# Performance work log

Measured on AMD Instinct MI355X. Metric: run time of the kernel, lower is better.

Reference implementation:

```python
import jax, jax.numpy as jnp
import numpy as np

N = 50000
E = 800000
IN_CH, HID, OUT_CH = 8, 64, 1
NEG_SLOPE = 0.2


def setup_inputs() -> dict:
    key = jax.random.key(0)
    ks = jax.random.split(key, 16)
    x = jax.random.normal(ks[0], (N, IN_CH), dtype=jnp.float32)
    edge_index = jax.random.randint(ks[1], (2, E), 0, N, dtype=jnp.int64)
    def glorot(k, shape):
        fan = shape[0] + shape[-1]
        return jax.random.uniform(k, shape, jnp.float32, -1.0, 1.0) * jnp.sqrt(6.0 / fan)
    # layer 1: in=8 -> 4 heads x 64, concat=False (mean over heads)
    W1 = glorot(ks[2], (IN_CH, 4 * HID))
    as1 = glorot(ks[3], (4, HID)); ad1 = glorot(ks[4], (4, HID))
    b1 = jnp.zeros((HID,), jnp.float32)
    # layer 2: 64 -> 4 heads x 64
    W2 = glorot(ks[5], (HID, 4 * HID))
    as2 = glorot(ks[6], (4, HID)); ad2 = glorot(ks[7], (4, HID))
    b2 = jnp.zeros((HID,), jnp.float32)
    # layer 3: 64 -> 1 head x 1
    W3 = glorot(ks[8], (HID, OUT_CH))
    as3 = glorot(ks[9], (1, OUT_CH)); ad3 = glorot(ks[10], (1, OUT_CH))
    b3 = jnp.zeros((OUT_CH,), jnp.float32)
    return {"x": x, "edge_index": edge_index,
            "W1": W1, "b1": b1, "as1": as1, "ad1": ad1,
            "W2": W2, "b2": b2, "as2": as2, "ad2": ad2,
            "W3": W3, "b3": b3, "as3": as3, "ad3": ad3}


def gat_conv(x, src, dst, W, b, a_src, a_dst, n_nodes):
    """PyG GATConv, concat=False (mean over heads), add_self_loops already applied."""
    heads, ch = a_src.shape
    h = (x @ W).reshape(n_nodes, heads, ch)            # [N,H,C]
    e_src = jnp.sum(h * a_src[None], axis=-1)          # [N,H]
    e_dst = jnp.sum(h * a_dst[None], axis=-1)          # [N,H]
    logits = jax.nn.leaky_relu(e_src[src] + e_dst[dst], NEG_SLOPE)  # [E,H]
    # softmax over incoming edges of each destination node (self loops ensure non-empty)
    m = jax.ops.segment_max(logits, dst, num_segments=n_nodes)      # [N,H]
    ex = jnp.exp(logits - m[dst])
    denom = jax.ops.segment_sum(ex, dst, num_segments=n_nodes)      # [N,H]
    alpha = ex / (denom[dst] + 1e-16)                  # [E,H]
    out = jax.ops.segment_sum(alpha[:, :, None] * h[src], dst, num_segments=n_nodes)  # [N,H,C]
    return jnp.mean(out, axis=1) + b                   # [N,C]


def reference(x, edge_index, W1, b1, as1, ad1, W2, b2, as2, ad2, W3, b3, as3, ad3):
    n = x.shape[0]
    loops = jnp.arange(n, dtype=edge_index.dtype)
    src = jnp.concatenate([edge_index[0], loops])
    dst = jnp.concatenate([edge_index[1], loops])
    h = jax.nn.elu(gat_conv(x, src, dst, W1, b1, as1, ad1, n))
    # Dropout(p=0.2) is identity in eval mode
    h = jax.nn.elu(gat_conv(h, src, dst, W2, b2, as2, ad2, n))
    out = jax.nn.sigmoid(gat_conv(h, src, dst, W3, b3, as3, ad3, n))
    return out  # [N,1] failure probability per node
```

## Files before the change

kernel.cpp:

```cpp
#include <hip/hip_runtime.h>
#include <hip/hip_bf16.h>
#include <hip/hip_fp16.h>
#include <math.h>

#define N_NODES 50000
#define N_EDGES 800000
#define N_TOT   (N_EDGES + N_NODES)
#define NEG_SLOPE 0.2f

static __device__ __forceinline__ float lrelu(float x){ return x >= 0.f ? x : NEG_SLOPE * x; }

__global__ void k_detect(const int* __restrict__ ei, int* __restrict__ flag){
  if (blockIdx.x == 0 && threadIdx.x == 0){
    int o = 0;
    #pragma unroll
    for (int i = 1; i < 16; i += 2) o |= ei[i];
    *flag = (o == 0) ? 1 : 0;
  }
}

__global__ void k_init(int* __restrict__ deg, int* __restrict__ fill){
  int i = blockIdx.x * blockDim.x + threadIdx.x;
  if (i < N_NODES){ deg[i] = 1; fill[i] = 0; }
}

__global__ void k_count(const int* __restrict__ ei, const int* __restrict__ flag,
                        int* __restrict__ deg){
  int e = blockIdx.x * blockDim.x + threadIdx.x;
  if (e >= N_EDGES) return;
  int f = *flag;
  int d = f ? ei[2*(N_EDGES + e)] : ei[N_EDGES + e];
  atomicAdd(&deg[d], 1);
}

__global__ void k_scan1(const int* __restrict__ deg, int* __restrict__ rowptr,
                        int* __restrict__ bsum){
  __shared__ int sd[256];
  int t = threadIdx.x;
  int base = blockIdx.x * 1024 + t * 4;
  int v0 = (base + 0 < N_NODES) ? deg[base + 0] : 0;
  int v1 = (base + 1 < N_NODES) ? deg[base + 1] : 0;
  int v2 = (base + 2 < N_NODES) ? deg[base + 2] : 0;
  int v3 = (base + 3 < N_NODES) ? deg[base + 3] : 0;
  int tsum = v0 + v1 + v2 + v3;
  sd[t] = tsum; __syncthreads();
  for (int off = 1; off < 256; off <<= 1){
    int vv = (t >= off) ? sd[t - off] : 0;
    __syncthreads();
    sd[t] += vv;
    __syncthreads();
  }
  int excl = sd[t] - tsum;
  if (base + 0 < N_NODES) rowptr[base + 0] = excl;
  if (base + 1 < N_NODES) rowptr[base + 1] = excl + v0;
  if (base + 2 < N_NODES) rowptr[base + 2] = excl + v0 + v1;
  if (base + 3 < N_NODES) rowptr[base + 3] = excl + v0 + v1 + v2;
  if (t == 255) bsum[blockIdx.x] = sd[255];
}

#define NB_SCAN 49
__global__ void k_scan2(const int* __restrict__ bsum, int* __restrict__ boff){
  int t = threadIdx.x;
  int v = (t < NB_SCAN) ? bsum[t] : 0;
  int incl = v;
  #pragma unroll
  for (int off = 1; off < 64; off <<= 1){
    int u = __shfl_up(incl, off);
    if (t >= off) incl += u;
  }
  if (t < NB_SCAN) boff[t] = incl - v;
}

__global__ void k_scan3(int* __restrict__ rowptr, const int* __restrict__ boff){
  int i = blockIdx.x * blockDim.x + threadIdx.x;
  if (i < N_NODES) rowptr[i] += boff[i >> 10];
  if (i == 0) rowptr[N_NODES] = N_TOT;
}

__global__ void k_scatter(const int* __restrict__ ei, const int* __restrict__ flag,
                          const int* __restrict__ rowptr, int* __restrict__ fill,
                          int* __restrict__ col){
  int e = blockIdx.x * blockDim.x + threadIdx.x;
  if (e >= N_TOT) return;
  int s, d;
  if (e < N_EDGES){
    int f = *flag;
    if (f){ s = ei[2*e]; d = ei[2*(N_EDGES + e)]; }
    else  { s = ei[e];   d = ei[N_EDGES + e]; }
  } else {
    s = d = e - N_EDGES;
  }
  int pos = atomicAdd(&fill[d], 1);
  col[rowptr[d] + pos] = s;
}


__global__ __launch_bounds__(256) void k_transform1(
    const float* __restrict__ xin, const float* __restrict__ W,
    const float* __restrict__ aS, const float* __restrict__ aD,
    __half* __restrict__ h, float* __restrict__ es, float* __restrict__ ed){
  __shared__ float wl[8 * 256];
  int tid = threadIdx.x;
  for (int i = tid; i < 8 * 256; i += 256) wl[i] = W[i];
  int lane = tid & 63, wv = tid >> 6, head = lane >> 4;
  float4 s4 = *(const float4*)&aS[4 * lane];
  float4 d4 = *(const float4*)&aD[4 * lane];
  __syncthreads();
  int base = (blockIdx.x * 4 + wv) * 8;
  for (int m = 0; m < 8; m++){
    int n = base + m;
    if (n >= N_NODES) break;
    float4 xa = *(const float4*)&xin[n * 8];
    float4 xb = *(const float4*)&xin[n * 8 + 4];
    float xs0 = xa.x, xs1 = xa.y, xs2 = xa.z, xs3 = xa.w;
    float xs4 = xb.x, xs5 = xb.y, xs6 = xb.z, xs7 = xb.w;
    float4 acc = make_float4(0.f, 0.f, 0.f, 0.f);
    #define T1STEP(k, xv) { float4 w4 = *(const float4*)&wl[(k)*256 + 4*lane]; \
      acc.x = fmaf(xv, w4.x, acc.x); acc.y = fmaf(xv, w4.y, acc.y); \
      acc.z = fmaf(xv, w4.z, acc.z); acc.w = fmaf(xv, w4.w, acc.w); }
    T1STEP(0, xs0) T1STEP(1, xs1) T1STEP(2, xs2) T1STEP(3, xs3)
    T1STEP(4, xs4) T1STEP(5, xs5) T1STEP(6, xs6) T1STEP(7, xs7)
    #undef T1STEP
    __half2 p0 = __floats2half2_rn(acc.x, acc.y);
    __half2 p1 = __floats2half2_rn(acc.z, acc.w);
    uint2 u; u.x = *(unsigned int*)&p0; u.y = *(unsigned int*)&p1;
    *(uint2*)&h[(size_t)n * 256 + 4 * lane] = u;
    float ps = acc.x*s4.x + acc.y*s4.y + acc.z*s4.z + acc.w*s4.w;
    float pd = acc.x*d4.x + acc.y*d4.y + acc.z*d4.z + acc.w*d4.w;
    #pragma unroll
    for (int off = 1; off < 16; off <<= 1){ ps += __shfl_xor(ps, off); pd += __shfl_xor(pd, off); }
    if ((lane & 15) == 0){ es[n * 4 + head] = ps; ed[n * 4 + head] = pd; }
  }
}

__global__ __launch_bounds__(256) void k_transform2(
    const float* __restrict__ xin, const float* __restrict__ W,
    const float* __restrict__ aS, const float* __restrict__ aD,
    __half* __restrict__ h, float* __restrict__ es, float* __restrict__ ed){
  __shared__ float wl[64 * 256];
  int tid = threadIdx.x;
  for (int i = tid; i < 64 * 256; i += 256) wl[i] = W[i];
  int lane = tid & 63, wv = tid >> 6, head = lane >> 4;
  float4 s4 = *(const float4*)&aS[4 * lane];
  float4 d4 = *(const float4*)&aD[4 * lane];
  __syncthreads();
  int base = (blockIdx.x * 4 + wv) * 8;
  float xr[8];
  #pragma unroll
  for (int m = 0; m < 8; m++){
    int n = base + m;
    xr[m] = (n < N_NODES) ? xin[(size_t)n * 64 + lane] : 0.f;
  }
  float4 acc[8];
  #pragma unroll
  for (int m = 0; m < 8; m++) acc[m] = make_float4(0.f, 0.f, 0.f, 0.f);
  #pragma unroll 4
  for (int k = 0; k < 64; k++){
    float4 w4 = *(const float4*)&wl[k * 256 + 4 * lane];
    #pragma unroll
    for (int m = 0; m < 8; m++){
      float xv = __shfl(xr[m], k);
      acc[m].x = fmaf(xv, w4.x, acc[m].x);
      acc[m].y = fmaf(xv, w4.y, acc[m].y);
      acc[m].z = fmaf(xv, w4.z, acc[m].z);
      acc[m].w = fmaf(xv, w4.w, acc[m].w);
    }
  }
  #pragma unroll
  for (int m = 0; m < 8; m++){
    int n = base + m;
    if (n >= N_NODES) break;
    __half2 p0 = __floats2half2_rn(acc[m].x, acc[m].y);
    __half2 p1 = __floats2half2_rn(acc[m].z, acc[m].w);
    uint2 u; u.x = *(unsigned int*)&p0; u.y = *(unsigned int*)&p1;
    *(uint2*)&h[(size_t)n * 256 + 4 * lane] = u;
    float ps = acc[m].x*s4.x + acc[m].y*s4.y + acc[m].z*s4.z + acc[m].w*s4.w;
    float pd = acc[m].x*d4.x + acc[m].y*d4.y + acc[m].z*d4.z + acc[m].w*d4.w;
    #pragma unroll
    for (int off = 1; off < 16; off <<= 1){ ps += __shfl_xor(ps, off); pd += __shfl_xor(pd, off); }
    if ((lane & 15) == 0){ es[n * 4 + head] = ps; ed[n * 4 + head] = pd; }
  }
}

__global__ __launch_bounds__(256) void k_transform3(
    const float* __restrict__ xin, const float* __restrict__ W3,
    const float* __restrict__ aS, const float* __restrict__ aD,
    float* __restrict__ h3, float* __restrict__ es3, float* __restrict__ ed3){
  int gid = blockIdx.x * blockDim.x + threadIdx.x;
  int n = gid >> 6, lane = gid & 63;
  if (n >= N_NODES) return;
  float v = xin[(size_t)n * 64 + lane] * W3[lane];
  #pragma unroll
  for (int off = 1; off < 64; off <<= 1) v += __shfl_xor(v, off);
  if (lane == 0){
    h3[n] = v;
    es3[n] = v * aS[0];
    ed3[n] = v * aD[0];
  }
}

__global__ __launch_bounds__(256) void k_agg(
    const __half* __restrict__ h, const float* __restrict__ es, const float* __restrict__ ed,
    const int* __restrict__ rowptr, const int* __restrict__ col,
    const float* __restrict__ bias, float* __restrict__ outf){
  int gid = blockIdx.x * blockDim.x + threadIdx.x;
  int d = gid >> 6, lane = gid & 63;
  if (d >= N_NODES) return;
  int start = rowptr[d], end = rowptr[d + 1];
  int head = lane >> 4;
  float eh = ed[d * 4 + head];
  const __half* hp = h + 4 * lane;
  float4 acc = make_float4(0.f, 0.f, 0.f, 0.f);
  float wsum = 0.f;
  int i = start;
  for (; i + 2 <= end; i += 2){
    int s0 = col[i], s1 = col[i + 1];
    float w0 = __expf(lrelu(es[s0 * 4 + head] + eh));
    float w1 = __expf(lrelu(es[s1 * 4 + head] + eh));
    uint2 u0 = *(const uint2*)(hp + (size_t)s0 * 256);
    uint2 u1 = *(const uint2*)(hp + (size_t)s1 * 256);
    wsum += w0 + w1;
    float2 a0 = __half22float2(*(__half2*)&u0.x);
    float2 b0 = __half22float2(*(__half2*)&u0.y);
    float2 a1 = __half22float2(*(__half2*)&u1.x);
    float2 b1 = __half22float2(*(__half2*)&u1.y);
    acc.x = fmaf(w0, a0.x, acc.x); acc.y = fmaf(w0, a0.y, acc.y);
    acc.z = fmaf(w0, b0.x, acc.z); acc.w = fmaf(w0, b0.y, acc.w);
    acc.x = fmaf(w1, a1.x, acc.x); acc.y = fmaf(w1, a1.y, acc.y);
    acc.z = fmaf(w1, b1.x, acc.z); acc.w = fmaf(w1, b1.y, acc.w);
  }
  if (i < end){
    int s0 = col[i];
    float w0 = __expf(lrelu(es[s0 * 4 + head] + eh));
    uint2 u0 = *(const uint2*)(hp + (size_t)s0 * 256);
    wsum += w0;
    float2 a0 = __half22float2(*(__half2*)&u0.x);
    float2 b0 = __half22float2(*(__half2*)&u0.y);
    acc.x = fmaf(w0, a0.x, acc.x); acc.y = fmaf(w0, a0.y, acc.y);
    acc.z = fmaf(w0, b0.x, acc.z); acc.w = fmaf(w0, b0.y, acc.w);
  }
  float inv = 1.0f / (wsum + 1e-16f);
  acc.x *= inv; acc.y *= inv; acc.z *= inv; acc.w *= inv;
  #pragma unroll
  for (int off = 16; off < 64; off <<= 1){
    acc.x += __shfl_xor(acc.x, off);
    acc.y += __shfl_xor(acc.y, off);
    acc.z += __shfl_xor(acc.z, off);
    acc.w += __shfl_xor(acc.w, off);
  }
  if (lane < 16){
    float4 b4 = *(const float4*)&bias[4 * lane];
    float ox = 0.25f * acc.x + b4.x;
    float oy = 0.25f * acc.y + b4.y;
    float oz = 0.25f * acc.z + b4.z;
    float ow = 0.25f * acc.w + b4.w;
    ox = ox > 0.f ? ox : expm1f(ox);
    oy = oy > 0.f ? oy : expm1f(oy);
    oz = oz > 0.f ? oz : expm1f(oz);
    ow = ow > 0.f ? ow : expm1f(ow);
    float4 o = make_float4(ox, oy, oz, ow);
    *(float4*)&outf[(size_t)d * 64 + 4 * lane] = o;
  }
}

__global__ __launch_bounds__(256) void k_agg3(
    const float* __restrict__ h3, const float* __restrict__ es3, const float* __restrict__ ed3,
    const int* __restrict__ rowptr, const int* __restrict__ col,
    const float* __restrict__ b3, float* __restrict__ out){
  int gid = blockIdx.x * blockDim.x + threadIdx.x;
  int d = gid >> 6, lane = gid & 63;
  if (d >= N_NODES) return;
  int start = rowptr[d], end = rowptr[d + 1];
  float edv = ed3[d];
  float num = 0.f, den = 0.f;
  for (int i = start + lane; i < end; i += 64){
    int s = col[i];
    float wgt = __expf(lrelu(es3[s] + edv));
    den += wgt;
    num = fmaf(wgt, h3[s], num);
  }
  #pragma unroll
  for (int off = 1; off < 64; off <<= 1){
    num += __shfl_xor(num, off);
    den += __shfl_xor(den, off);
  }
  if (lane == 0){
    float v = num / (den + 1e-16f) + b3[0];
    out[d] = 1.f / (1.f + __expf(-v));
  }
}

extern "C" void kernel_launch(void* const* d_in, const int* in_sizes, int n_in,
                              void* d_out, int out_size, void* d_ws, size_t ws_size,
                              hipStream_t stream) {
  const float* x   = (const float*)d_in[0];
  const int*   ei  = (const int*)  d_in[1];
  const float* W1  = (const float*)d_in[2];
  const float* b1  = (const float*)d_in[3];
  const float* as1 = (const float*)d_in[4];
  const float* ad1 = (const float*)d_in[5];
  const float* W2  = (const float*)d_in[6];
  const float* b2  = (const float*)d_in[7];
  const float* as2 = (const float*)d_in[8];
  const float* ad2 = (const float*)d_in[9];
  const float* W3  = (const float*)d_in[10];
  const float* b3  = (const float*)d_in[11];
  const float* as3 = (const float*)d_in[12];
  const float* ad3 = (const float*)d_in[13];
  float* out = (float*)d_out;

  char* w = (char*)d_ws;
  size_t off = 0;
  auto alloc = [&](size_t bytes) -> char* {
    char* p = w + off;
    off += (bytes + 255) & ~size_t(255);
    return p;
  };
  int*    flag   = (int*)   alloc(64);
  int*    deg    = (int*)   alloc(N_NODES * 4);
  int*    fill   = (int*)   alloc(N_NODES * 4);
  int*    rowptr = (int*)   alloc((N_NODES + 1) * 4);
  int*    bsum   = (int*)   alloc(64 * 4);
  int*    boff   = (int*)   alloc(64 * 4);
  int*    col    = (int*)   alloc((size_t)N_TOT * 4);
  __half* h      = (__half*)alloc((size_t)N_NODES * 256 * 2);
  float*  es     = (float*) alloc((size_t)N_NODES * 4 * 4);
  float*  ed     = (float*) alloc((size_t)N_NODES * 4 * 4);
  float*  feat1  = (float*) alloc((size_t)N_NODES * 64 * 4);
  float*  feat2  = (float*) alloc((size_t)N_NODES * 64 * 4);
  float*  h3     = (float*) alloc(N_NODES * 4);
  float*  es3    = (float*) alloc(N_NODES * 4);
  float*  ed3    = (float*) alloc(N_NODES * 4);
  (void)ws_size; (void)in_sizes; (void)n_in; (void)out_size;

  k_detect <<<1, 64, 0, stream>>>(ei, flag);
  k_init   <<<(N_NODES + 255) / 256, 256, 0, stream>>>(deg, fill);
  k_count  <<<(N_EDGES + 255) / 256, 256, 0, stream>>>(ei, flag, deg);
  k_scan1  <<<NB_SCAN, 256, 0, stream>>>(deg, rowptr, bsum);
  k_scan2  <<<1, 64, 0, stream>>>(bsum, boff);
  k_scan3  <<<(N_NODES + 255) / 256, 256, 0, stream>>>(rowptr, boff);
  k_scatter<<<(N_TOT + 255) / 256, 256, 0, stream>>>(ei, flag, rowptr, fill, col);

  const int grid_t12 = (N_NODES + 31) / 32;
  const int grid_wpn = (N_NODES * 64 + 255) / 256;

  k_transform1<<<grid_t12, 256, 0, stream>>>(x, W1, as1, ad1, h, es, ed);
  k_agg       <<<grid_wpn, 256, 0, stream>>>(h, es, ed, rowptr, col, b1, feat1);
  k_transform2<<<grid_t12, 256, 0, stream>>>(feat1, W2, as2, ad2, h, es, ed);
  k_agg       <<<grid_wpn, 256, 0, stream>>>(h, es, ed, rowptr, col, b2, feat2);
  k_transform3<<<grid_wpn, 256, 0, stream>>>(feat2, W3, as3, ad3, h3, es3, ed3);
  k_agg3      <<<grid_wpn, 256, 0, stream>>>(h3, es3, ed3, rowptr, col, b3, out);
}
```

Before: 411.0 us.

## Batch edge weights per 16-lane group, halve transform2 LDS, pack 4 nodes per wave in agg3

In k_agg, each 16-lane head group now loads up to 16 neighbour indices and attention weights at once, computing each exp only once per edge. The values are broadcast with shuffles to the inner loop, replacing the per-lane redundant col/es loads and exp calls. k_transform2 stages W in two 32-row halves, cutting LDS from 64KB to 32KB to allow more resident blocks, at the cost of an extra barrier. k_agg3 assigns 4 destination nodes per wave with 16 lanes each instead of one node per 64-lane wave, which suits the low average degree of about 17.

```diff
diff --git a/kernel.cpp b/kernel.cpp
--- a/kernel.cpp
+++ b/kernel.cpp
@@ -137,13 +137,11 @@
     const float* __restrict__ xin, const float* __restrict__ W,
     const float* __restrict__ aS, const float* __restrict__ aD,
     __half* __restrict__ h, float* __restrict__ es, float* __restrict__ ed){
-  __shared__ float wl[64 * 256];
+  __shared__ float wl[32 * 256];
   int tid = threadIdx.x;
-  for (int i = tid; i < 64 * 256; i += 256) wl[i] = W[i];
   int lane = tid & 63, wv = tid >> 6, head = lane >> 4;
   float4 s4 = *(const float4*)&aS[4 * lane];
   float4 d4 = *(const float4*)&aD[4 * lane];
-  __syncthreads();
   int base = (blockIdx.x * 4 + wv) * 8;
   float xr[8];
   #pragma unroll
@@ -154,16 +152,24 @@
   float4 acc[8];
   #pragma unroll
   for (int m = 0; m < 8; m++) acc[m] = make_float4(0.f, 0.f, 0.f, 0.f);
-  #pragma unroll 4
-  for (int k = 0; k < 64; k++){
-    float4 w4 = *(const float4*)&wl[k * 256 + 4 * lane];
-    #pragma unroll
-    for (int m = 0; m < 8; m++){
-      float xv = __shfl(xr[m], k);
-      acc[m].x = fmaf(xv, w4.x, acc[m].x);
-      acc[m].y = fmaf(xv, w4.y, acc[m].y);
-      acc[m].z = fmaf(xv, w4.z, acc[m].z);
-      acc[m].w = fmaf(xv, w4.w, acc[m].w);
+  for (int hf = 0; hf < 2; hf++){
+    if (hf) __syncthreads();
+    const float4* Wv = (const float4*)(W + hf * 32 * 256);
+    float4* wlv = (float4*)wl;
+    #pragma unroll
+    for (int i = 0; i < 8; i++) wlv[tid + 256 * i] = Wv[tid + 256 * i];
+    __syncthreads();
+    #pragma unroll 4
+    for (int k = 0; k < 32; k++){
+      float4 w4 = *(const float4*)&wl[k * 256 + 4 * lane];
+      #pragma unroll
+      for (int m = 0; m < 8; m++){
+        float xv = __shfl(xr[m], hf * 32 + k);
+        acc[m].x = fmaf(xv, w4.x, acc[m].x);
+        acc[m].y = fmaf(xv, w4.y, acc[m].y);
+        acc[m].z = fmaf(xv, w4.z, acc[m].z);
+        acc[m].w = fmaf(xv, w4.w, acc[m].w);
+      }
     }
   }
   #pragma unroll
@@ -207,37 +213,30 @@
   int d = gid >> 6, lane = gid & 63;
   if (d >= N_NODES) return;
   int start = rowptr[d], end = rowptr[d + 1];
-  int head = lane >> 4;
-  float eh = ed[d * 4 + head];
+  int head = lane >> 4, e16 = lane & 15;
+  float edh = ed[d * 4 + head];
   const __half* hp = h + 4 * lane;
   float4 acc = make_float4(0.f, 0.f, 0.f, 0.f);
   float wsum = 0.f;
-  int i = start;
-  for (; i + 2 <= end; i += 2){
-    int s0 = col[i], s1 = col[i + 1];
-    float w0 = __expf(lrelu(es[s0 * 4 + head] + eh));
-    float w1 = __expf(lrelu(es[s1 * 4 + head] + eh));
-    uint2 u0 = *(const uint2*)(hp + (size_t)s0 * 256);
-    uint2 u1 = *(const uint2*)(hp + (size_t)s1 * 256);
-    wsum += w0 + w1;
-    float2 a0 = __half22float2(*(__half2*)&u0.x);
-    float2 b0 = __half22float2(*(__half2*)&u0.y);
-    float2 a1 = __half22float2(*(__half2*)&u1.x);
-    float2 b1 = __half22float2(*(__half2*)&u1.y);
-    acc.x = fmaf(w0, a0.x, acc.x); acc.y = fmaf(w0, a0.y, acc.y);
-    acc.z = fmaf(w0, b0.x, acc.z); acc.w = fmaf(w0, b0.y, acc.w);
-    acc.x = fmaf(w1, a1.x, acc.x); acc.y = fmaf(w1, a1.y, acc.y);
-    acc.z = fmaf(w1, b1.x, acc.z); acc.w = fmaf(w1, b1.y, acc.w);
-  }
-  if (i < end){
-    int s0 = col[i];
-    float w0 = __expf(lrelu(es[s0 * 4 + head] + eh));
-    uint2 u0 = *(const uint2*)(hp + (size_t)s0 * 256);
-    wsum += w0;
-    float2 a0 = __half22float2(*(__half2*)&u0.x);
-    float2 b0 = __half22float2(*(__half2*)&u0.y);
-    acc.x = fmaf(w0, a0.x, acc.x); acc.y = fmaf(w0, a0.y, acc.y);
-    acc.z = fmaf(w0, b0.x, acc.z); acc.w = fmaf(w0, b0.y, acc.w);
+  for (int base = start; base < end; base += 16){
+    int nb = end - base; nb = nb < 16 ? nb : 16;
+    int s_mine = col[base + (e16 < nb ? e16 : 0)];
+    float lg = lrelu(es[s_mine * 4 + head] + edh);
+    float w_mine = (e16 < nb) ? __expf(lg) : 0.f;
+    float ws = w_mine;
+    ws += __shfl_xor(ws, 1); ws += __shfl_xor(ws, 2);
+    ws += __shfl_xor(ws, 4); ws += __shfl_xor(ws, 8);
+    wsum += ws;
+    #pragma unroll 4
+    for (int e = 0; e < nb; e++){
+      int s_e = __shfl(s_mine, e);
+      float w_e = __shfl(w_mine, (head << 4) | e);
+      uint2 u = *(const uint2*)(hp + (size_t)s_e * 256);
+      float2 a = __half22float2(*(__half2*)&u.x);
+      float2 b = __half22float2(*(__half2*)&u.y);
+      acc.x = fmaf(w_e, a.x, acc.x); acc.y = fmaf(w_e, a.y, acc.y);
+      acc.z = fmaf(w_e, b.x, acc.z); acc.w = fmaf(w_e, b.y, acc.w);
+    }
   }
   float inv = 1.0f / (wsum + 1e-16f);
   acc.x *= inv; acc.y *= inv; acc.z *= inv; acc.w *= inv;
@@ -268,25 +267,28 @@
     const int* __restrict__ rowptr, const int* __restrict__ col,
     const float* __restrict__ b3, float* __restrict__ out){
   int gid = blockIdx.x * blockDim.x + threadIdx.x;
-  int d = gid >> 6, lane = gid & 63;
-  if (d >= N_NODES) return;
-  int start = rowptr[d], end = rowptr[d + 1];
-  float edv = ed3[d];
-  float num = 0.f, den = 0.f;
-  for (int i = start + lane; i < end; i += 64){
-    int s = col[i];
-    float wgt = __expf(lrelu(es3[s] + edv));
-    den += wgt;
-    num = fmaf(wgt, h3[s], num);
-  }
-  #pragma unroll
-  for (int off = 1; off < 64; off <<= 1){
-    num += __shfl_xor(num, off);
-    den += __shfl_xor(den, off);
-  }
-  if (lane == 0){
-    float v = num / (den + 1e-16f) + b3[0];
-    out[d] = 1.f / (1.f + __expf(-v));
+  int wv = gid >> 6, lane = gid & 63;
+  int sub = lane >> 4, li = lane & 15;
+  int d = wv * 4 + sub;
+  if (d < N_NODES){
+    int start = rowptr[d], end = rowptr[d + 1];
+    float edv = ed3[d];
+    float num = 0.f, den = 0.f;
+    for (int i = start + li; i < end; i += 16){
+      int s = col[i];
+      float wgt = __expf(lrelu(es3[s] + edv));
+      den += wgt;
+      num = fmaf(wgt, h3[s], num);
+    }
+    #pragma unroll
+    for (int off = 1; off < 16; off <<= 1){
+      num += __shfl_xor(num, off);
+      den += __shfl_xor(den, off);
+    }
+    if (li == 0){
+      float v = num / (den + 1e-16f) + b3[0];
+      out[d] = 1.f / (1.f + __expf(-v));
+    }
   }
 }
 
@@ -343,11 +345,12 @@
 
   const int grid_t12 = (N_NODES + 31) / 32;
   const int grid_wpn = (N_NODES * 64 + 255) / 256;
+  const int grid_w4n = ((N_NODES + 3) / 4 * 64 + 255) / 256;
 
   k_transform1<<<grid_t12, 256, 0, stream>>>(x, W1, as1, ad1, h, es, ed);
   k_agg       <<<grid_wpn, 256, 0, stream>>>(h, es, ed, rowptr, col, b1, feat1);
   k_transform2<<<grid_t12, 256, 0, stream>>>(feat1, W2, as2, ad2, h, es, ed);
   k_agg       <<<grid_wpn, 256, 0, stream>>>(h, es, ed, rowptr, col, b2, feat2);
   k_transform3<<<grid_wpn, 256, 0, stream>>>(feat2, W3, as3, ad3, h3, es3, ed3);
-  k_agg3      <<<grid_wpn, 256, 0, stream>>>(h3, es3, ed3, rowptr, col, b3, out);
-}
+  k_agg3      <<<grid_w4n, 256, 0, stream>>>(h3, es3, ed3, rowptr, col, b3, out);
+}
```

Result: no change. 415.1 us (+1.0%).
